# Kernel optimization log

Measured on AMD Instinct MI355X. Metric: run time of the kernel, lower is better.

Reference implementation:

```python
import jax, jax.numpy as jnp
import numpy as np

S = 16          # state_dim
H = 96          # hidden_dim
A = 64          # num_actions
B = 256         # batch_size
D_IN = S * S * 64      # 16384
D_H = H * H            # 9216
SPLIT = D_H - S * S    # 8960, action/selection split point


def setup_inputs() -> dict:
    key = jax.random.key(0)
    ks = jax.random.split(key, 14)
    s = jax.random.normal(ks[0], (B, S, S, 64), dtype=jnp.float32)
    mask = jax.random.randint(ks[1], (B, S, S), 0, 2).astype(bool)
    u = jax.random.uniform(ks[2], (B, S * S), dtype=jnp.float32,
                           minval=1e-6, maxval=1.0 - 1e-6)
    def lin(k, fin, fout):
        kw, kb = jax.random.split(k)
        sc = 1.0 / np.sqrt(fin)
        return (jax.random.uniform(kw, (fin, fout), minval=-sc, maxval=sc, dtype=jnp.float32),
                jax.random.uniform(kb, (fout,), minval=-sc, maxval=sc, dtype=jnp.float32))
    W1, b1 = lin(ks[3], D_IN, D_H)
    W2, b2 = lin(ks[4], D_H, D_H)
    W3, b3 = lin(ks[5], D_H, D_H)
    Wa, ba = lin(ks[6], SPLIT, A)
    Ws, bs = lin(ks[7], S * S, S * S)
    return {"s": s, "mask": mask, "u": u, "W1": W1, "b1": b1, "W2": W2,
            "b2": b2, "W3": W3, "b3": b3, "Wa": Wa, "ba": ba, "Ws": Ws, "bs": bs}


def reference(s, mask, u, W1, b1, W2, b2, W3, b3, Wa, ba, Ws, bs):
    x = s.reshape(s.shape[0], -1).astype(jnp.float32)        # [B, D_IN]
    x = jax.nn.relu(x @ W1 + b1)                             # [B, D_H]
    x = jax.nn.relu(x @ W2 + b2)
    x = jax.nn.relu(x @ W3 + b3)
    x_action = jax.nn.softmax(x[:, :SPLIT] @ Wa + ba, axis=1)  # [B, A]
    # selection branch
    p = jax.nn.softmax(x[:, SPLIT:] @ Ws + bs, axis=1)         # [B, S*S]
    m = mask.reshape(mask.shape[0], -1)                        # [B, S*S]
    p = jnp.where(m, -1e9, p)        # masked_fill on the probs (faithful)
    p = jax.nn.softmax(p, axis=1)
    # parallel Gumbel-max == Categorical over valid (unnormalized) probs
    gumbel = -jnp.log(-jnp.log(u))
    scores = jnp.where(m, -jnp.inf, jnp.log(p) + gumbel)
    idx = jnp.argmax(scores, axis=1)                           # [B]
    coordinate = jnp.stack([idx // S, idx % S], axis=1)        # [B, 2]
    sel_prob = jnp.take_along_axis(p, idx[:, None], axis=1)    # [B, 1]
    final_action_prob = x_action * sel_prob                    # [B, A]
    return final_action_prob, coordinate
```

## Files before the change

kernel.cpp:

```cpp
#include <hip/hip_runtime.h>
#include <hip/hip_fp16.h>


typedef _Float16 f16;
typedef _Float16 f16x4 __attribute__((ext_vector_type(4)));
typedef _Float16 f16x8 __attribute__((ext_vector_type(8)));
typedef float f32x4 __attribute__((ext_vector_type(4)));

#define DH 9216
#define SPLIT 8960

__device__ __forceinline__ void gload16(const void* g, void* l) {
    __builtin_amdgcn_global_load_lds(
        (const __attribute__((address_space(1))) void*)g,
        (__attribute__((address_space(3))) void*)l, 16, 0, 0);
}

__device__ __forceinline__ size_t pk_off(int row, int k) {
    int tk = k >> 5, q = (k >> 3) & 3;
    int mhalf = row >> 7, wmA = (row >> 6) & 1, ri = (row >> 4) & 3, lc = row & 15;
    int h = (wmA << 8) | (ri << 6) | (q << 4) | lc;
    return (size_t)(tk * 2 + mhalf) * 8192 + (size_t)h * 16;
}

__global__ void cvt_kernel(const float* __restrict__ in, char* __restrict__ outp) {
    int idx = blockIdx.x * blockDim.x + threadIdx.x;
    int row = idx >> 11;
    int k8  = (idx & 2047) << 3;
    const float* src = in + ((size_t)row << 14) + k8;
    f16x8 h;
#pragma unroll
    for (int j = 0; j < 8; ++j) h[j] = (_Float16)src[j];
    *(f16x8*)(outp + pk_off(row, k8)) = h;
}

__global__ __launch_bounds__(256, 3) void gemm_kernel(
    const char* __restrict__ Ap, int K, int Kh, int yshift,
    const float* __restrict__ W,
    f16* __restrict__ P)
{
    __shared__ __align__(16) char lds[2][24576];
    const int bid  = blockIdx.x;
    const int y    = bid & ((1 << yshift) - 1);
    const int rem  = bid >> yshift;
    const int m0   = (rem & 1) << 7;
    const int n0   = (rem >> 1) << 7;
    const int tid  = threadIdx.x;
    const int lane = tid & 63;
    const int wid  = tid >> 6;
    const int wm   = wid >> 1, wn = wid & 1;
    const int kbase = y * Kh;
    const int ns   = Kh >> 5;

    f32x4 acc[4][4] = {};

    const float* wsrc0;
    const float* wsrc1;
    const float* wsrc2;
    const float* wsrc3;
    {
        int g0 = tid,      k0 = g0 >> 5, c0 = (g0 & 31) ^ ((5 * (k0 >> 3)) & 31);
        int g1 = tid + 256, k1 = g1 >> 5, c1 = (g1 & 31) ^ ((5 * (k1 >> 3)) & 31);
        int g2 = tid + 512, k2 = g2 >> 5, c2 = (g2 & 31) ^ ((5 * (k2 >> 3)) & 31);
        int g3 = tid + 768, k3 = g3 >> 5, c3 = (g3 & 31) ^ ((5 * (k3 >> 3)) & 31);
        wsrc0 = W + (size_t)(kbase + k0) * DH + n0 + (c0 << 2);
        wsrc1 = W + (size_t)(kbase + k1) * DH + n0 + (c1 << 2);
        wsrc2 = W + (size_t)(kbase + k2) * DH + n0 + (c2 << 2);
        wsrc3 = W + (size_t)(kbase + k3) * DH + n0 + (c3 << 2);
    }
    const char* ap = Ap + (size_t)(y * (Kh >> 5) * 2 + (m0 >> 7)) * 8192;

    auto issue = [&](int slot) {
        char* dst = &lds[slot][0];
        gload16(wsrc0, dst + (size_t)tid * 16);          wsrc0 += 32 * DH;
        gload16(wsrc1, dst + (size_t)(tid + 256) * 16);  wsrc1 += 32 * DH;
        gload16(wsrc2, dst + (size_t)(tid + 512) * 16);  wsrc2 += 32 * DH;
        gload16(wsrc3, dst + (size_t)(tid + 768) * 16);  wsrc3 += 32 * DH;
        gload16(ap + (size_t)tid * 16,        dst + 16384 + (size_t)tid * 16);
        gload16(ap + (size_t)tid * 16 + 4096, dst + 16384 + (size_t)tid * 16 + 4096);
        ap += 16384;
    };

    const int q  = lane >> 4;
    const int lc = lane & 15;
    auto step = [&](int slot) {
        const float* wl = (const float*)&lds[slot][0];
        const f16*   al = (const f16*)&lds[slot][16384];
        f16x8 af[4], bf[4];
#pragma unroll
        for (int ri = 0; ri < 4; ++ri)
            af[ri] = *(const f16x8*)(al + (((wm << 8) + (ri << 6) + lane) << 3));
        const int wbase = (q << 10) + (lc & 3);
#pragma unroll
        for (int ni = 0; ni < 4; ++ni) {
            int p = ((wn << 4) + (ni << 2) + (lc >> 2)) ^ (5 * q);
            int fi = wbase + ((p & 31) << 2);
            f16x8 b;
#pragma unroll
            for (int j = 0; j < 8; ++j)
                b[j] = (_Float16)wl[fi + (j << 7)];
            bf[ni] = b;
        }
#pragma unroll
        for (int ri = 0; ri < 4; ++ri)
#pragma unroll
            for (int ni = 0; ni < 4; ++ni)
                acc[ri][ni] = __builtin_amdgcn_mfma_f32_16x16x32_f16(
                    af[ri], bf[ni], acc[ri][ni], 0, 0, 0);
    };

    issue(0);
    issue(1);
    __builtin_amdgcn_sched_barrier(0);

    for (int t = 0; t < ns; ++t) {
        if (t + 1 < ns) asm volatile("s_waitcnt vmcnt(6)" ::: "memory");
        else            asm volatile("s_waitcnt vmcnt(0)" ::: "memory");
        __builtin_amdgcn_sched_barrier(0);
        __builtin_amdgcn_s_barrier();
        __builtin_amdgcn_sched_barrier(0);
        step(t & 1);
        __builtin_amdgcn_sched_barrier(0);
        asm volatile("s_waitcnt lgkmcnt(0)" ::: "memory");
        __builtin_amdgcn_sched_barrier(0);
        __builtin_amdgcn_s_barrier();
        __builtin_amdgcn_sched_barrier(0);
        if (t + 2 < ns) {
            issue(t & 1);
            __builtin_amdgcn_sched_barrier(0);
        }
    }

    f16* Pb = P + (size_t)y * (256 * DH);
#pragma unroll
    for (int ri = 0; ri < 4; ++ri) {
        int row = m0 + wm * 64 + ri * 16 + (q << 2);
#pragma unroll
        for (int ni = 0; ni < 4; ++ni) {
            int col = n0 + wn * 64 + ni * 16 + lc;
#pragma unroll
            for (int rg = 0; rg < 4; ++rg)
                Pb[(size_t)(row + rg) * DH + col] = (_Float16)acc[ri][ni][rg];
        }
    }
}

__global__ __launch_bounds__(256) void reduce_kernel(
    const f16* __restrict__ P, int S,
    const float* __restrict__ bias,
    char* __restrict__ ohp, float* __restrict__ out32) {
    const size_t n = 256 * DH;
    const size_t i = ((size_t)blockIdx.x * 256 + threadIdx.x) * 8;
    if (i >= n) return;
    const int row = (int)(i / DH);
    const int d   = (int)(i % DH);
    float r[8];
    {
        float4 b0 = *(const float4*)(bias + d);
        float4 b1 = *(const float4*)(bias + d + 4);
        r[0] = b0.x; r[1] = b0.y; r[2] = b0.z; r[3] = b0.w;
        r[4] = b1.x; r[5] = b1.y; r[6] = b1.z; r[7] = b1.w;
    }
    for (int j = 0; j < S; ++j) {
        f16x8 v = *(const f16x8*)(P + (size_t)j * n + i);
#pragma unroll
        for (int e = 0; e < 8; ++e) r[e] += (float)v[e];
    }
#pragma unroll
    for (int e = 0; e < 8; ++e) r[e] = fmaxf(r[e], 0.f);
    if (ohp) {
        f16x8 h;
#pragma unroll
        for (int e = 0; e < 8; ++e) h[e] = (_Float16)r[e];
        *(f16x8*)(ohp + pk_off(row, d)) = h;
    }
    if (out32) {
        float4 o0 = {r[0], r[1], r[2], r[3]};
        float4 o1 = {r[4], r[5], r[6], r[7]};
        *(float4*)(out32 + i) = o0;
        *(float4*)(out32 + i + 4) = o1;
    }
}

__global__ __launch_bounds__(256) void action_kernel(
    const float* __restrict__ X3, const float* __restrict__ Wa,
    const float* __restrict__ ba, float* __restrict__ xact) {
    __shared__ float xs[SPLIT];
    __shared__ float red[256];
    const int row = blockIdx.x, t = threadIdx.x;
    const float* xr = X3 + (size_t)row * DH;
    for (int k = t * 4; k < SPLIT; k += 1024)
        *(float4*)&xs[k] = *(const float4*)(xr + k);
    __syncthreads();
    const int col = t & 63, kqq = t >> 6;
    float acc = 0.f;
    for (int k = kqq * 2240; k < (kqq + 1) * 2240; ++k)
        acc += xs[k] * Wa[(size_t)k * 64 + col];
    red[t] = acc;
    __syncthreads();
    if (t < 64) {
        float z = red[t] + red[t + 64] + red[t + 128] + red[t + 192] + ba[t];
        float mx = z;
        for (int off = 32; off; off >>= 1) mx = fmaxf(mx, __shfl_xor(mx, off));
        float e = expf(z - mx);
        float s = e;
        for (int off = 32; off; off >>= 1) s += __shfl_xor(s, off);
        xact[row * 64 + t] = e / s;
    }
}

__global__ __launch_bounds__(256) void select_kernel(
    const float* __restrict__ X3, const float* __restrict__ Ws,
    const float* __restrict__ bs, const void* __restrict__ maskp,
    const float* __restrict__ u, const float* __restrict__ xact,
    float* __restrict__ out) {
    __shared__ float xs[256];
    __shared__ float psh[256];
    __shared__ float rr[4];
    __shared__ float bestv[4];
    __shared__ int besti[4];
    __shared__ int sIdx;
    __shared__ int smode;
    const int row = blockIdx.x, t = threadIdx.x;
    const int lane = t & 63, wid = t >> 6;

    if (t < 64) {
        unsigned v = ((const unsigned*)maskp)[t];
        int okInt  = __all(v <= 1u);
        int okByte = __all((v & 0xFEFEFEFEu) == 0u);
        if (t == 0) smode = okInt ? 0 : (okByte ? 1 : 2);
    }
    xs[t] = X3[(size_t)row * DH + SPLIT + t];
    __syncthreads();

    bool mk;
    if (smode == 0)       mk = ((const int*)maskp)[row * 256 + t] != 0;
    else if (smode == 1)  mk = ((const unsigned char*)maskp)[row * 256 + t] != 0;
    else                  mk = ((const float*)maskp)[row * 256 + t] != 0.0f;

    float z = bs[t];
    for (int k = 0; k < 256; ++k)
        z += xs[k] * Ws[k * 256 + t];

    float v = z;
    for (int off = 32; off; off >>= 1) v = fmaxf(v, __shfl_xor(v, off));
    if (lane == 0) rr[wid] = v;
    __syncthreads();
    float m1 = fmaxf(fmaxf(rr[0], rr[1]), fmaxf(rr[2], rr[3]));
    __syncthreads();
    float e1 = expf(z - m1);
    v = e1;
    for (int off = 32; off; off >>= 1) v += __shfl_xor(v, off);
    if (lane == 0) rr[wid] = v;
    __syncthreads();
    float s1 = rr[0] + rr[1] + rr[2] + rr[3];
    __syncthreads();
    float p1 = e1 / s1;

    float q = mk ? -1e9f : p1;
    v = q;
    for (int off = 32; off; off >>= 1) v = fmaxf(v, __shfl_xor(v, off));
    if (lane == 0) rr[wid] = v;
    __syncthreads();
    float m2 = fmaxf(fmaxf(rr[0], rr[1]), fmaxf(rr[2], rr[3]));
    __syncthreads();
    float e2 = expf(q - m2);
    v = e2;
    for (int off = 32; off; off >>= 1) v += __shfl_xor(v, off);
    if (lane == 0) rr[wid] = v;
    __syncthreads();
    float s2 = rr[0] + rr[1] + rr[2] + rr[3];
    float p2 = e2 / s2;
    psh[t] = p2;

    float g = -logf(-logf(u[row * 256 + t]));
    float sc = mk ? -INFINITY : (logf(p2) + g);
    float bv = sc;
    int bi = t;
    for (int off = 32; off; off >>= 1) {
        float ov = __shfl_xor(bv, off);
        int oi = __shfl_xor(bi, off);
        if (ov > bv || (ov == bv && oi < bi)) { bv = ov; bi = oi; }
    }
    if (lane == 0) { bestv[wid] = bv; besti[wid] = bi; }
    __syncthreads();
    if (t == 0) {
        float fv = bestv[0];
        int fi = besti[0];
        for (int w = 1; w < 4; ++w)
            if (bestv[w] > fv || (bestv[w] == fv && besti[w] < fi)) {
                fv = bestv[w]; fi = besti[w];
            }
        sIdx = fi;
    }
    __syncthreads();
    const int idx = sIdx;
    const float sp = psh[idx];
    if (t < 64) out[row * 64 + t] = xact[row * 64 + t] * sp;
    if (t == 0) {
        out[256 * 64 + row * 2 + 0] = (float)(idx >> 4);
        out[256 * 64 + row * 2 + 1] = (float)(idx & 15);
    }
}

extern "C" void kernel_launch(void* const* d_in, const int* in_sizes, int n_in,
                              void* d_out, int out_size, void* d_ws, size_t ws_size,
                              hipStream_t stream) {
    const float* s  = (const float*)d_in[0];
    const void*  mask = d_in[1];
    const float* u  = (const float*)d_in[2];
    const float* W1 = (const float*)d_in[3];
    const float* b1 = (const float*)d_in[4];
    const float* W2 = (const float*)d_in[5];
    const float* b2 = (const float*)d_in[6];
    const float* W3 = (const float*)d_in[7];
    const float* b3 = (const float*)d_in[8];
    const float* Wa = (const float*)d_in[9];
    const float* ba = (const float*)d_in[10];
    const float* Ws = (const float*)d_in[11];
    const float* bs = (const float*)d_in[12];
    float* out = (float*)d_out;
    char* ws = (char*)d_ws;

    char*  A0p = ws + 0;
    char*  X1p = ws + 8388608;
    char*  X2p = ws + 0;
    float* X3  = (float*)(ws + 13107200);
    float* XA  = (float*)(ws + 22544384);
    f16*   P   = (f16*)(ws + 22609920);

    const size_t pbytes = 4718592ull;
    int yshift = (ws_size >= 22609920ull + 8 * pbytes) ? 3 : 2;
    const int S = 1 << yshift;

    cvt_kernel<<<2048, 256, 0, stream>>>(s, A0p);

    const int nblk = (2 * 72) << yshift;
    gemm_kernel<<<nblk, 256, 0, stream>>>(A0p, 16384, 16384 / S, yshift, W1, P);
    reduce_kernel<<<1152, 256, 0, stream>>>(P, S, b1, X1p, nullptr);
    gemm_kernel<<<nblk, 256, 0, stream>>>(X1p, DH, DH / S, yshift, W2, P);
    reduce_kernel<<<1152, 256, 0, stream>>>(P, S, b2, X2p, nullptr);
    gemm_kernel<<<nblk, 256, 0, stream>>>(X2p, DH, DH / S, yshift, W3, P);
    reduce_kernel<<<1152, 256, 0, stream>>>(P, S, b3, nullptr, X3);

    action_kernel<<<256, 256, 0, stream>>>(X3, Wa, ba, XA);
    select_kernel<<<256, 256, 0, stream>>>(X3, Ws, bs, mask, u, XA, out);
}
```

Baseline: 514.4 us.

## Retile GEMM to full-M 256x64 blocks so each weight element is fetched once

Each GEMM block now covers all 256 batch rows and a 64-column slice of the weight, replacing the earlier 128x128 tile split across two M halves. The fp32 weight matrix, the dominant memory traffic, is therefore loaded from global memory once instead of twice, while the small fp16 activation tile is loaded by every block. The block count stays the same. LDS layout, swizzle and fragment addressing are rewritten to match. Each wave now covers 64 rows by 64 columns. The trade-off is more activation traffic per block.

```diff
diff --git a/kernel.cpp b/kernel.cpp
--- a/kernel.cpp
+++ b/kernel.cpp
@@ -42,13 +42,10 @@
     __shared__ __align__(16) char lds[2][24576];
     const int bid  = blockIdx.x;
     const int y    = bid & ((1 << yshift) - 1);
-    const int rem  = bid >> yshift;
-    const int m0   = (rem & 1) << 7;
-    const int n0   = (rem >> 1) << 7;
+    const int n0   = (bid >> yshift) << 6;
     const int tid  = threadIdx.x;
     const int lane = tid & 63;
-    const int wid  = tid >> 6;
-    const int wm   = wid >> 1, wn = wid & 1;
+    const int wm   = tid >> 6;
     const int kbase = y * Kh;
     const int ns   = Kh >> 5;
 
@@ -56,28 +53,22 @@
 
     const float* wsrc0;
     const float* wsrc1;
-    const float* wsrc2;
-    const float* wsrc3;
     {
-        int g0 = tid,      k0 = g0 >> 5, c0 = (g0 & 31) ^ ((5 * (k0 >> 3)) & 31);
-        int g1 = tid + 256, k1 = g1 >> 5, c1 = (g1 & 31) ^ ((5 * (k1 >> 3)) & 31);
-        int g2 = tid + 512, k2 = g2 >> 5, c2 = (g2 & 31) ^ ((5 * (k2 >> 3)) & 31);
-        int g3 = tid + 768, k3 = g3 >> 5, c3 = (g3 & 31) ^ ((5 * (k3 >> 3)) & 31);
+        int g0 = tid,       k0 = g0 >> 4, c0 = (g0 & 15) ^ ((5 * (k0 >> 3)) & 15);
+        int g1 = tid + 256, k1 = g1 >> 4, c1 = (g1 & 15) ^ ((5 * (k1 >> 3)) & 15);
         wsrc0 = W + (size_t)(kbase + k0) * DH + n0 + (c0 << 2);
         wsrc1 = W + (size_t)(kbase + k1) * DH + n0 + (c1 << 2);
-        wsrc2 = W + (size_t)(kbase + k2) * DH + n0 + (c2 << 2);
-        wsrc3 = W + (size_t)(kbase + k3) * DH + n0 + (c3 << 2);
-    }
-    const char* ap = Ap + (size_t)(y * (Kh >> 5) * 2 + (m0 >> 7)) * 8192;
+    }
+    const char* ap = Ap + (size_t)(y * (Kh >> 5) * 2) * 8192;
 
     auto issue = [&](int slot) {
         char* dst = &lds[slot][0];
         gload16(wsrc0, dst + (size_t)tid * 16);          wsrc0 += 32 * DH;
         gload16(wsrc1, dst + (size_t)(tid + 256) * 16);  wsrc1 += 32 * DH;
-        gload16(wsrc2, dst + (size_t)(tid + 512) * 16);  wsrc2 += 32 * DH;
-        gload16(wsrc3, dst + (size_t)(tid + 768) * 16);  wsrc3 += 32 * DH;
-        gload16(ap + (size_t)tid * 16,        dst + 16384 + (size_t)tid * 16);
-        gload16(ap + (size_t)tid * 16 + 4096, dst + 16384 + (size_t)tid * 16 + 4096);
+        gload16(ap + (size_t)tid * 16,         dst + 8192 + (size_t)tid * 16);
+        gload16(ap + (size_t)tid * 16 + 4096,  dst + 8192 + (size_t)tid * 16 + 4096);
+        gload16(ap + (size_t)tid * 16 + 8192,  dst + 8192 + (size_t)tid * 16 + 8192);
+        gload16(ap + (size_t)tid * 16 + 12288, dst + 8192 + (size_t)tid * 16 + 12288);
         ap += 16384;
     };
 
@@ -85,20 +76,21 @@
     const int lc = lane & 15;
     auto step = [&](int slot) {
         const float* wl = (const float*)&lds[slot][0];
-        const f16*   al = (const f16*)&lds[slot][16384];
+        const f16*   al = (const f16*)&lds[slot][8192];
         f16x8 af[4], bf[4];
+        const int abase = ((wm >> 1) << 9) + ((wm & 1) << 8) + lane;
 #pragma unroll
         for (int ri = 0; ri < 4; ++ri)
-            af[ri] = *(const f16x8*)(al + (((wm << 8) + (ri << 6) + lane) << 3));
-        const int wbase = (q << 10) + (lc & 3);
+            af[ri] = *(const f16x8*)(al + (size_t)((abase + (ri << 6)) << 3));
+        const int s5 = (5 * q) & 15;
 #pragma unroll
         for (int ni = 0; ni < 4; ++ni) {
-            int p = ((wn << 4) + (ni << 2) + (lc >> 2)) ^ (5 * q);
-            int fi = wbase + ((p & 31) << 2);
+            int c = (ni << 4) + lc;
+            int fi = (q << 9) + ((((c >> 2) ^ s5) & 15) << 2) + (c & 3);
             f16x8 b;
 #pragma unroll
             for (int j = 0; j < 8; ++j)
-                b[j] = (_Float16)wl[fi + (j << 7)];
+                b[j] = (_Float16)wl[fi + (j << 6)];
             bf[ni] = b;
         }
 #pragma unroll
@@ -134,10 +126,10 @@
     f16* Pb = P + (size_t)y * (256 * DH);
 #pragma unroll
     for (int ri = 0; ri < 4; ++ri) {
-        int row = m0 + wm * 64 + ri * 16 + (q << 2);
+        int row = wm * 64 + ri * 16 + (q << 2);
 #pragma unroll
         for (int ni = 0; ni < 4; ++ni) {
-            int col = n0 + wn * 64 + ni * 16 + lc;
+            int col = n0 + ni * 16 + lc;
 #pragma unroll
             for (int rg = 0; rg < 4; ++rg)
                 Pb[(size_t)(row + rg) * DH + col] = (_Float16)acc[ri][ni][rg];
@@ -335,7 +327,7 @@
 
     cvt_kernel<<<2048, 256, 0, stream>>>(s, A0p);
 
-    const int nblk = (2 * 72) << yshift;
+    const int nblk = 144 << yshift;
     gemm_kernel<<<nblk, 256, 0, stream>>>(A0p, 16384, 16384 / S, yshift, W1, P);
     reduce_kernel<<<1152, 256, 0, stream>>>(P, S, b1, X1p, nullptr);
     gemm_kernel<<<nblk, 256, 0, stream>>>(X1p, DH, DH / S, yshift, W2, P);
```

Result: slower. 535.1 us (+4.0%).
